# Kernel tuning notes

Measured on AMD Instinct MI355X. Metric: run time of the kernel, lower is better.

The kernel has to match this reference:

```python
import jax, jax.numpy as jnp
import numpy as np

B = 4096          # number of graphs in the batch
D = 256           # ORB node feature dim (out_dim)
AVG_NODES = 128   # average nodes per graph
N_TOTAL = B * AVG_NODES


def setup_inputs() -> dict:
    key = jax.random.key(0)
    # Ragged per-graph node counts that sum exactly to N_TOTAL.
    rng = np.random.default_rng(0)
    counts = rng.multinomial(N_TOTAL, np.full(B, 1.0 / B))  # ~128 each, all >0 w.h.p.
    n_nodes = jnp.asarray(counts, dtype=jnp.int32)
    node_feats = jax.random.normal(key, (N_TOTAL, D), dtype=jnp.float32)
    return {"node_feats": node_feats, "n_nodes": n_nodes}


def reference(node_feats, n_nodes):
    # Fused segment-mean: one pass over nodes instead of B small kernels.
    n_total = node_feats.shape[0]
    b = n_nodes.shape[0]
    # segment id for every node: [0,0,...,1,1,...,B-1,...]
    seg_ids = jnp.repeat(jnp.arange(b, dtype=jnp.int32), n_nodes,
                         total_repeat_length=n_total)
    sums = jax.ops.segment_sum(node_feats, seg_ids, num_segments=b)  # (B, D)
    graph_feats = sums / n_nodes[:, None].astype(node_feats.dtype)
    return graph_feats
```

## Files before the change

kernel.cpp:

```cpp
#include <hip/hip_runtime.h>


#define BLOCK 256
#define GPB 4

typedef float f4 __attribute__((ext_vector_type(4)));

__global__ __launch_bounds__(BLOCK) void seg_mean_fused(
    const float* __restrict__ feats,
    const int* __restrict__ n_nodes,
    float* __restrict__ out) {
  __shared__ int red[BLOCK];
  __shared__ int offs[GPB];

  const int t = threadIdx.x;
  const int g0 = blockIdx.x * GPB;

  int s = 0;
  for (int i = t; i < g0; i += BLOCK) s += n_nodes[i];
  red[t] = s;
  __syncthreads();
#pragma unroll
  for (int d = BLOCK / 2; d > 0; d >>= 1) {
    if (t < d) red[t] += red[t + d];
    __syncthreads();
  }
  if (t == 0) {
    int o = red[0];
#pragma unroll
    for (int j = 0; j < GPB; ++j) {
      offs[j] = o;
      o += n_nodes[g0 + j];
    }
  }
  __syncthreads();

  const int wave = t >> 6;
  const int lane = t & 63;
  const int g = g0 + wave;
  const int n = n_nodes[g];
  const int start = offs[wave];

  const f4* __restrict__ src =
      reinterpret_cast<const f4*>(feats) + (size_t)start * 64 + lane;

  f4 acc[8];
#pragma unroll
  for (int i = 0; i < 8; ++i) acc[i] = (f4)0.0f;

  int r = 0;
  for (; r + 8 <= n; r += 8) {
#pragma unroll
    for (int i = 0; i < 8; ++i) {
      acc[i] += __builtin_nontemporal_load(&src[(size_t)(r + i) * 64]);
    }
  }
  for (; r < n; ++r) acc[0] += __builtin_nontemporal_load(&src[(size_t)r * 64]);

  f4 total = ((acc[0] + acc[1]) + (acc[2] + acc[3])) +
             ((acc[4] + acc[5]) + (acc[6] + acc[7]));
  total *= (1.0f / (float)n);

  __builtin_nontemporal_store(
      total, &reinterpret_cast<f4*>(out)[(size_t)g * 64 + lane]);
}

extern "C" void kernel_launch(void* const* d_in, const int* in_sizes, int n_in,
                              void* d_out, int out_size, void* d_ws, size_t ws_size,
                              hipStream_t stream) {
  const float* node_feats = (const float*)d_in[0];
  const int* n_nodes = (const int*)d_in[1];
  float* out = (float*)d_out;

  const int b = in_sizes[1];
  seg_mean_fused<<<b / GPB, BLOCK, 0, stream>>>(node_feats, n_nodes, out);
}
```

Baseline: 646.1 us.

## Precompute segment offsets in a separate scan kernel and software-pipeline loads

```diff
diff --git a/kernel.cpp b/kernel.cpp
--- a/kernel.cpp
+++ b/kernel.cpp
@@ -6,40 +6,46 @@
 
 typedef float f4 __attribute__((ext_vector_type(4)));
 
-__global__ __launch_bounds__(BLOCK) void seg_mean_fused(
+__global__ __launch_bounds__(BLOCK) void seg_offsets(
+    const int* __restrict__ n_nodes, int* __restrict__ offs, int b) {
+  __shared__ int part[BLOCK];
+  const int t = threadIdx.x;
+  const int vpt = (b + BLOCK - 1) / BLOCK;
+  const int lo = t * vpt;
+  const int hi = min(b, lo + vpt);
+
+  int s = 0;
+  for (int i = lo; i < hi; ++i) s += n_nodes[i];
+  part[t] = s;
+  __syncthreads();
+
+  for (int d = 1; d < BLOCK; d <<= 1) {
+    int v = (t >= d) ? part[t - d] : 0;
+    __syncthreads();
+    part[t] += v;
+    __syncthreads();
+  }
+
+  int base = (t == 0) ? 0 : part[t - 1];
+  for (int i = lo; i < hi; ++i) {
+    offs[i] = base;
+    base += n_nodes[i];
+  }
+}
+
+__global__ __launch_bounds__(BLOCK) void seg_mean(
     const float* __restrict__ feats,
     const int* __restrict__ n_nodes,
-    float* __restrict__ out) {
-  __shared__ int red[BLOCK];
-  __shared__ int offs[GPB];
-
+    const int* __restrict__ offs,
+    float* __restrict__ out, int b) {
   const int t = threadIdx.x;
-  const int g0 = blockIdx.x * GPB;
-
-  int s = 0;
-  for (int i = t; i < g0; i += BLOCK) s += n_nodes[i];
-  red[t] = s;
-  __syncthreads();
-#pragma unroll
-  for (int d = BLOCK / 2; d > 0; d >>= 1) {
-    if (t < d) red[t] += red[t + d];
-    __syncthreads();
-  }
-  if (t == 0) {
-    int o = red[0];
-#pragma unroll
-    for (int j = 0; j < GPB; ++j) {
-      offs[j] = o;
-      o += n_nodes[g0 + j];
-    }
-  }
-  __syncthreads();
-
   const int wave = t >> 6;
   const int lane = t & 63;
-  const int g = g0 + wave;
+  const int g = blockIdx.x * GPB + wave;
+  if (g >= b) return;
+
   const int n = n_nodes[g];
-  const int start = offs[wave];
+  const int start = offs[g];
 
   const f4* __restrict__ src =
       reinterpret_cast<const f4*>(feats) + (size_t)start * 64 + lane;
@@ -49,20 +55,30 @@
   for (int i = 0; i < 8; ++i) acc[i] = (f4)0.0f;
 
   int r = 0;
-  for (; r + 8 <= n; r += 8) {
+  if (n >= 16) {
+    f4 buf[8];
 #pragma unroll
-    for (int i = 0; i < 8; ++i) {
-      acc[i] += __builtin_nontemporal_load(&src[(size_t)(r + i) * 64]);
+    for (int i = 0; i < 8; ++i) buf[i] = src[(size_t)i * 64];
+
+    for (r = 8; r + 8 <= n; r += 8) {
+      f4 nb[8];
+#pragma unroll
+      for (int i = 0; i < 8; ++i) nb[i] = src[(size_t)(r + i) * 64];
+#pragma unroll
+      for (int i = 0; i < 8; ++i) acc[i] += buf[i];
+#pragma unroll
+      for (int i = 0; i < 8; ++i) buf[i] = nb[i];
     }
+#pragma unroll
+    for (int i = 0; i < 8; ++i) acc[i] += buf[i];
   }
-  for (; r < n; ++r) acc[0] += __builtin_nontemporal_load(&src[(size_t)r * 64]);
+  for (; r < n; ++r) acc[0] += src[(size_t)r * 64];
 
   f4 total = ((acc[0] + acc[1]) + (acc[2] + acc[3])) +
              ((acc[4] + acc[5]) + (acc[6] + acc[7]));
   total *= (1.0f / (float)n);
 
-  __builtin_nontemporal_store(
-      total, &reinterpret_cast<f4*>(out)[(size_t)g * 64 + lane]);
+  reinterpret_cast<f4*>(out)[(size_t)g * 64 + lane] = total;
 }
 
 extern "C" void kernel_launch(void* const* d_in, const int* in_sizes, int n_in,
@@ -71,7 +87,11 @@
   const float* node_feats = (const float*)d_in[0];
   const int* n_nodes = (const int*)d_in[1];
   float* out = (float*)d_out;
+  int* offs = (int*)d_ws;
 
   const int b = in_sizes[1];
-  seg_mean_fused<<<b / GPB, BLOCK, 0, stream>>>(node_feats, n_nodes, out);
+
+  seg_offsets<<<1, BLOCK, 0, stream>>>(n_nodes, offs, b);
+  seg_mean<<<(b + GPB - 1) / GPB, BLOCK, 0, stream>>>(node_feats, n_nodes, offs,
+                                                      out, b);
 }
```

Result: slower. 686.3 us (+6.2%).
